# Kernel optimization log

Hardware: AMD Instinct MI355X
Metric: run time of the kernel (lower is better)

Reference implementation:

```python
import jax, jax.numpy as jnp
import numpy as np

D_MODEL = 1024; N_HEAD = 16; HD = 64
D_STATE = 128; D_CONV = 4; EXPAND = 2; HEADDIM = 64
D_INNER = EXPAND * D_MODEL          # 2048
NHEADS = D_INNER // HEADDIM         # 32
FFN = 4 * D_MODEL                   # 4096
B, T = 2, 1024


def rmsnorm(x, eps=1e-6):
    # FastSimpleRMSNorm: no learnable weight
    return x * jax.lax.rsqrt(jnp.mean(x * x, axis=-1, keepdims=True) + eps)


def causal_dwconv(x, w, b):
    # x: (..., T, C), w: (C, K), b: (C,). Causal depthwise conv (left pad K-1).
    K = w.shape[1]
    t = x.shape[-2]
    pad = [(0, 0)] * (x.ndim - 2) + [(K - 1, 0), (0, 0)]
    xp = jnp.pad(x, pad)
    y = jnp.zeros_like(x) + b
    for k in range(K):
        y = y + w[:, k] * jax.lax.slice_in_dim(xp, k, k + t, axis=-2)
    return y


def block_forward(x, W_in, conv_w, conv_b, A_log, Dm, dt_bias, mnorm_w, W_out,
                  W_qkv, W_cproj, qconv_w, qconv_b, kconv_w, kconv_b, vconv_w, vconv_b,
                  time_maa_k, time_maa_r, W_key, W_rec, W_val):
    Bsz, Tn, _ = x.shape
    # ---- Mamba2 branch ----
    h = rmsnorm(x)
    zxbcdt = h @ W_in                                  # (B,T,2*D_INNER+2*N+H)
    z = zxbcdt[..., :D_INNER]
    xBC = zxbcdt[..., D_INNER:2 * D_INNER + 2 * D_STATE]
    dt = zxbcdt[..., -NHEADS:]
    xBC = jax.nn.silu(causal_dwconv(xBC, conv_w, conv_b))
    xm = xBC[..., :D_INNER]
    Bm = xBC[..., D_INNER:D_INNER + D_STATE]           # (B,T,N)
    Cm = xBC[..., -D_STATE:]                           # (B,T,N)
    dt = jax.nn.softplus(dt + dt_bias)                 # (B,T,H)
    A = -jnp.exp(A_log)                                # (H,)
    xh = xm.reshape(Bsz, Tn, NHEADS, HEADDIM)          # (B,T,H,P)

    def step(hstate, inp):
        dt_t, x_t, B_t, C_t = inp                      # (B,H),(B,H,P),(B,N),(B,N)
        dA = jnp.exp(dt_t * A)                         # (B,H)
        hstate = hstate * dA[..., None, None] + (dt_t[..., None] * x_t)[..., None] * B_t[:, None, None, :]
        y_t = jnp.einsum('bhpn,bn->bhp', hstate, C_t)
        return hstate, y_t

    h0 = jnp.zeros((Bsz, NHEADS, HEADDIM, D_STATE), x.dtype)
    _, ys = jax.lax.scan(step, h0, (jnp.swapaxes(dt, 0, 1), jnp.swapaxes(xh, 0, 1),
                                    jnp.swapaxes(Bm, 0, 1), jnp.swapaxes(Cm, 0, 1)))
    y = jnp.swapaxes(ys, 0, 1) + xh * Dm[:, None]      # (B,T,H,P)
    y = y.reshape(Bsz, Tn, D_INNER) * jax.nn.silu(z)   # gated
    y = y * jax.lax.rsqrt(jnp.mean(y * y, axis=-1, keepdims=True) + 1e-5) * mnorm_w
    x = x + y @ W_out

    # ---- MQA with depthwise convs ----
    h = rmsnorm(x)
    qkv = h @ W_qkv                                    # (B,T,D_MODEL+2*HD)
    q = qkv[..., :D_MODEL].reshape(Bsz, Tn, N_HEAD, HD).transpose(0, 2, 1, 3)  # (B,H,T,D)
    k = qkv[..., D_MODEL:D_MODEL + HD]                 # (B,T,D) single kv head
    v = qkv[..., -HD:]
    q = causal_dwconv(q, qconv_w, qconv_b)
    k = causal_dwconv(k, kconv_w, kconv_b)
    v = causal_dwconv(v, vconv_w, vconv_b)
    scores = jnp.einsum('bhtd,bsd->bhts', q, k) / np.float32(np.sqrt(HD))
    mask = jnp.tril(jnp.ones((Tn, Tn), bool))
    scores = jnp.where(mask, scores, -jnp.inf)
    p = jax.nn.softmax(scores, axis=-1)
    y = jnp.einsum('bhts,bsd->bhtd', p, v)
    y = y.transpose(0, 2, 1, 3).reshape(Bsz, Tn, D_MODEL)
    x = x + y @ W_cproj

    # ---- RWKV CMix FFN ----
    h = rmsnorm(x)
    xx = jnp.pad(h, ((0, 0), (1, 0), (0, 0)))[:, :Tn] - h   # time_shift(x) - x
    xk = h + xx * time_maa_k
    xr = h + xx * time_maa_r
    kf = jnp.square(jax.nn.relu(xk @ W_key))           # ReLU^2
    kv = kf @ W_val
    x = x + jax.nn.sigmoid(xr @ W_rec) * kv
    return x


def setup_inputs() -> dict:
    key = jax.random.key(0)
    ks = jax.random.split(key, 16)
    def w(k, shape, sc=0.02):
        return jax.random.normal(k, shape, jnp.float32) * sc
    x = jax.random.normal(ks[0], (B, T, D_MODEL), jnp.float32)
    W_in = w(ks[1], (D_MODEL, 2 * D_INNER + 2 * D_STATE + NHEADS))
    conv_w = w(ks[2], (D_INNER + 2 * D_STATE, D_CONV), 0.2)
    conv_b = jnp.zeros((D_INNER + 2 * D_STATE,), jnp.float32)
    A_log = jnp.log(jnp.arange(1, NHEADS + 1, dtype=jnp.float32))
    Dm = jnp.ones((NHEADS,), jnp.float32)
    dt_bias = w(ks[3], (NHEADS,), 0.5)
    mnorm_w = jnp.ones((D_INNER,), jnp.float32)
    W_out = w(ks[4], (D_INNER, D_MODEL))
    W_qkv = w(ks[5], (D_MODEL, D_MODEL + 2 * HD))
    W_cproj = w(ks[6], (D_MODEL, D_MODEL))
    qconv_w = w(ks[7], (HD, 3), 0.3); qconv_b = jnp.zeros((HD,), jnp.float32)
    kconv_w = w(ks[8], (HD, 3), 0.3); kconv_b = jnp.zeros((HD,), jnp.float32)
    vconv_w = w(ks[9], (HD, 3), 0.3); vconv_b = jnp.zeros((HD,), jnp.float32)
    ddd = jnp.arange(D_MODEL, dtype=jnp.float32) / D_MODEL
    time_maa_k = 1.0 - ddd  # layer_id=0 -> ratio_1_to_almost0 = 1
    time_maa_r = 1.0 - ddd
    W_key = w(ks[10], (D_MODEL, FFN))
    W_rec = w(ks[11], (D_MODEL, D_MODEL))
    W_val = w(ks[12], (FFN, D_MODEL))
    return dict(x=x, W_in=W_in, conv_w=conv_w, conv_b=conv_b, A_log=A_log, Dm=Dm,
                dt_bias=dt_bias, mnorm_w=mnorm_w, W_out=W_out, W_qkv=W_qkv, W_cproj=W_cproj,
                qconv_w=qconv_w, qconv_b=qconv_b, kconv_w=kconv_w, kconv_b=kconv_b,
                vconv_w=vconv_w, vconv_b=vconv_b, time_maa_k=time_maa_k, time_maa_r=time_maa_r,
                W_key=W_key, W_rec=W_rec, W_val=W_val)


def reference(x, W_in, conv_w, conv_b, A_log, Dm, dt_bias, mnorm_w, W_out,
              W_qkv, W_cproj, qconv_w, qconv_b, kconv_w, kconv_b, vconv_w, vconv_b,
              time_maa_k, time_maa_r, W_key, W_rec, W_val):
    return block_forward(x, W_in, conv_w, conv_b, A_log, Dm, dt_bias, mnorm_w, W_out,
                         W_qkv, W_cproj, qconv_w, qconv_b, kconv_w, kconv_b, vconv_w, vconv_b,
                         time_maa_k, time_maa_r, W_key, W_rec, W_val)
```

## Files before the change

### kernel.cpp

```cpp
#include <hip/hip_runtime.h>
#include <hip/hip_bf16.h>
#include <math.h>

#define BB 2
#define TT 1024
#define BT (BB*TT)
#define DM 1024
#define DI 2048
#define DS 128
#define NHS 32
#define PDIM 64
#define NHA 16
#define HD 64
#define FFN_ 4096
#define NZX 4384
#define NXBC 2304
#define NXBCD 2336
#define CL 128
#define NC 8

typedef __hip_bfloat16 bf16;
typedef short bf16x8 __attribute__((ext_vector_type(8)));
typedef float f32x4 __attribute__((ext_vector_type(4)));

__device__ __forceinline__ float b2f(bf16 v){ return __bfloat162float(v); }
__device__ __forceinline__ bf16 f2b(float v){ return __float2bfloat16(v); }

__device__ __forceinline__ void gload16(const void* g, void* l) {
  __builtin_amdgcn_global_load_lds(
      (const __attribute__((address_space(1))) unsigned int*)g,
      (__attribute__((address_space(3))) unsigned int*)l,
      16, 0, 0);
}

__global__ void k_rms_in(const float* __restrict__ xin, float* __restrict__ X,
                         bf16* __restrict__ H) {
  int row = blockIdx.x;
  int tid = threadIdx.x;
  const float* xr = xin + (size_t)row * DM;
  float v[4]; float ss = 0.f;
  #pragma unroll
  for (int i = 0; i < 4; ++i) { v[i] = xr[tid*4+i]; ss += v[i]*v[i]; }
  __shared__ float red[256];
  red[tid] = ss; __syncthreads();
  for (int s = 128; s > 0; s >>= 1) { if (tid < s) red[tid] += red[tid+s]; __syncthreads(); }
  float scale = rsqrtf(red[0]/(float)DM + 1e-6f);
  float* Xr = X + (size_t)row*DM; bf16* Hr = H + (size_t)row*DM;
  #pragma unroll
  for (int i = 0; i < 4; ++i) { Xr[tid*4+i] = v[i]; Hr[tid*4+i] = f2b(v[i]*scale); }
}

__global__ void k_rms_f32(const float* __restrict__ X, bf16* __restrict__ H) {
  int row = blockIdx.x;
  int tid = threadIdx.x;
  const float* xr = X + (size_t)row * DM;
  float v[4]; float ss = 0.f;
  #pragma unroll
  for (int i = 0; i < 4; ++i) { v[i] = xr[tid*4+i]; ss += v[i]*v[i]; }
  __shared__ float red[256];
  red[tid] = ss; __syncthreads();
  for (int s = 128; s > 0; s >>= 1) { if (tid < s) red[tid] += red[tid+s]; __syncthreads(); }
  float scale = rsqrtf(red[0]/(float)DM + 1e-6f);
  bf16* Hr = H + (size_t)row*DM;
  #pragma unroll
  for (int i = 0; i < 4; ++i) Hr[tid*4+i] = f2b(v[i]*scale);
}

__global__ void k_rms_shift(const float* __restrict__ X, const float* __restrict__ maak,
                            const float* __restrict__ maar,
                            bf16* __restrict__ XK, bf16* __restrict__ XR) {
  int row = blockIdx.x; int t = row & (TT - 1);
  int tid = threadIdx.x;
  const float* xr = X + (size_t)row*DM;
  const float* xp = xr - DM;
  float v[4], pv[4]; float ss = 0.f, ssp = 0.f;
  #pragma unroll
  for (int i = 0; i < 4; ++i) {
    int c = tid*4 + i;
    v[i] = xr[c]; ss += v[i]*v[i];
    pv[i] = (t > 0) ? xp[c] : 0.f; ssp += pv[i]*pv[i];
  }
  __shared__ float red[256], red2[256];
  red[tid] = ss; red2[tid] = ssp; __syncthreads();
  for (int s = 128; s > 0; s >>= 1) {
    if (tid < s) { red[tid] += red[tid+s]; red2[tid] += red2[tid+s]; }
    __syncthreads();
  }
  float scale  = rsqrtf(red[0]/(float)DM + 1e-6f);
  float scalep = (t > 0) ? rsqrtf(red2[0]/(float)DM + 1e-6f) : 0.f;
  bf16* xk = XK + (size_t)row*DM; bf16* xrw = XR + (size_t)row*DM;
  #pragma unroll
  for (int i = 0; i < 4; ++i) {
    int c = tid*4 + i;
    float h = v[i]*scale;
    float xx = pv[i]*scalep - h;
    xk[c]  = f2b(h + xx*maak[c]);
    xrw[c] = f2b(h + xx*maar[c]);
  }
}

__global__ void k_tcast(const float* __restrict__ W, bf16* __restrict__ Wt,
                        int K, int N) {
  __shared__ float t[32][33];
  int tx = threadIdx.x, ty = threadIdx.y;
  int n0 = blockIdx.x*32, k0 = blockIdx.y*32;
  #pragma unroll
  for (int i = 0; i < 4; ++i) {
    int k = k0 + ty + i*8, n = n0 + tx;
    t[ty + i*8][tx] = (n < N) ? W[(size_t)k*N + n] : 0.f;
  }
  __syncthreads();
  #pragma unroll
  for (int i = 0; i < 4; ++i) {
    int n = n0 + ty + i*8, k = k0 + tx;
    Wt[(size_t)n*K + k] = f2b(t[tx][ty + i*8]);
  }
}

template<int EPI, bool ADD, bool OUTBF>
__global__ __launch_bounds__(256)
void mfma_gemm(const bf16* __restrict__ A, const bf16* __restrict__ Bt,
               float* __restrict__ C, bf16* __restrict__ Cbf,
               int M, int N, int K) {
  __shared__ bf16 As[128*32];
  __shared__ bf16 Bs[128*32];
  int tid = threadIdx.x;
  int wave = tid >> 6, lane = tid & 63;
  int m_l = lane & 15, quad = lane >> 4;
  int wr = (wave & 1) * 64, wc = (wave >> 1) * 64;
  int row0 = blockIdx.y * 128, col0 = blockIdx.x * 128;
  f32x4 acc[4][4];
  #pragma unroll
  for (int i = 0; i < 4; ++i)
    #pragma unroll
    for (int j = 0; j < 4; ++j) acc[i][j] = (f32x4){0.f,0.f,0.f,0.f};
  int lr = lane >> 2;
  int lc = (lane & 3) * 8;
  for (int k0 = 0; k0 < K; k0 += 32) {
    __syncthreads();
    #pragma unroll
    for (int g = 0; g < 2; ++g) {
      int rbase = 32*wave + 16*g;
      gload16(&A [(size_t)(row0 + rbase + lr)*K + k0 + lc], &As[rbase*32]);
      gload16(&Bt[(size_t)(col0 + rbase + lr)*K + k0 + lc], &Bs[rbase*32]);
    }
    __syncthreads();
    bf16x8 af[4], bfv[4];
    #pragma unroll
    for (int i = 0; i < 4; ++i) af[i]  = *(const bf16x8*)&As[(wr + i*16 + m_l)*32 + quad*8];
    #pragma unroll
    for (int j = 0; j < 4; ++j) bfv[j] = *(const bf16x8*)&Bs[(wc + j*16 + m_l)*32 + quad*8];
    #pragma unroll
    for (int i = 0; i < 4; ++i)
      #pragma unroll
      for (int j = 0; j < 4; ++j)
        acc[i][j] = __builtin_amdgcn_mfma_f32_16x16x32_bf16(af[i], bfv[j], acc[i][j], 0, 0, 0);
  }
  #pragma unroll
  for (int i = 0; i < 4; ++i) {
    #pragma unroll
    for (int j = 0; j < 4; ++j) {
      int col = col0 + wc + j*16 + m_l;
      if (col < N) {
        #pragma unroll
        for (int r = 0; r < 4; ++r) {
          int row = row0 + wr + i*16 + quad*4 + r;
          float v = acc[i][j][r];
          if (EPI == 1) { v = fmaxf(v, 0.f); v = v*v; }
          else if (EPI == 2) v = 1.f/(1.f + __expf(-v));
          if (OUTBF)      Cbf[(size_t)row*N + col] = f2b(v);
          else if (ADD)   C[(size_t)row*N + col] += v;
          else            C[(size_t)row*N + col]  = v;
        }
      }
    }
  }
}

__global__ __launch_bounds__(256)
void mfma_sk32(const bf16* __restrict__ A, const bf16* __restrict__ Bt,
               float* __restrict__ P0, float* __restrict__ P1,
               float* __restrict__ P2, float* __restrict__ P3,
               int M, int N, int K, int kchunk) {
  __shared__ bf16 As[128*32];
  __shared__ bf16 Bs[128*32];
  int tid = threadIdx.x;
  int wave = tid >> 6, lane = tid & 63;
  int m_l = lane & 15, quad = lane >> 4;
  int wr = (wave & 1) * 64, wc = (wave >> 1) * 64;
  int row0 = blockIdx.y * 128, col0 = blockIdx.x * 128;
  int kbeg = blockIdx.z * kchunk;
  int kend = kbeg + kchunk;
  f32x4 acc[4][4];
  #pragma unroll
  for (int i = 0; i < 4; ++i)
    #pragma unroll
    for (int j = 0; j < 4; ++j) acc[i][j] = (f32x4){0.f,0.f,0.f,0.f};
  int lr = lane >> 2;
  int lc = (lane & 3) * 8;
  for (int k0 = kbeg; k0 < kend; k0 += 32) {
    __syncthreads();
    #pragma unroll
    for (int g = 0; g < 2; ++g) {
      int rbase = 32*wave + 16*g;
      gload16(&A [(size_t)(row0 + rbase + lr)*K + k0 + lc], &As[rbase*32]);
      gload16(&Bt[(size_t)(col0 + rbase + lr)*K + k0 + lc], &Bs[rbase*32]);
    }
    __syncthreads();
    bf16x8 af[4], bfv[4];
    #pragma unroll
    for (int i = 0; i < 4; ++i) af[i]  = *(const bf16x8*)&As[(wr + i*16 + m_l)*32 + quad*8];
    #pragma unroll
    for (int j = 0; j < 4; ++j) bfv[j] = *(const bf16x8*)&Bs[(wc + j*16 + m_l)*32 + quad*8];
    #pragma unroll
    for (int i = 0; i < 4; ++i)
      #pragma unroll
      for (int j = 0; j < 4; ++j)
        acc[i][j] = __builtin_amdgcn_mfma_f32_16x16x32_bf16(af[i], bfv[j], acc[i][j], 0, 0, 0);
  }
  float* P = (blockIdx.z == 0) ? P0 : (blockIdx.z == 1) ? P1 : (blockIdx.z == 2) ? P2 : P3;
  #pragma unroll
  for (int i = 0; i < 4; ++i) {
    #pragma unroll
    for (int j = 0; j < 4; ++j) {
      int col = col0 + wc + j*16 + m_l;
      if (col < N) {
        #pragma unroll
        for (int r = 0; r < 4; ++r) {
          int row = row0 + wr + i*16 + quad*4 + r;
          P[(size_t)row*N + col] = acc[i][j][r];
        }
      }
    }
  }
}

template<int Z, int EPI, bool ADD>
__global__ void k_reduce(float* __restrict__ dst, const float* __restrict__ p0,
                         const float* __restrict__ p1, const float* __restrict__ p2,
                         const float* __restrict__ p3) {
  size_t i = ((size_t)blockIdx.x*256 + threadIdx.x)*4;
  float4 a = *(const float4*)(p0 + i);
  float4 b = *(const float4*)(p1 + i);
  float r0 = a.x + b.x, r1 = a.y + b.y, r2 = a.z + b.z, r3 = a.w + b.w;
  if (Z == 4) {
    float4 c = *(const float4*)(p2 + i);
    float4 d = *(const float4*)(p3 + i);
    r0 += c.x + d.x; r1 += c.y + d.y; r2 += c.z + d.z; r3 += c.w + d.w;
  }
  if (EPI == 2) {
    r0 = 1.f/(1.f + __expf(-r0)); r1 = 1.f/(1.f + __expf(-r1));
    r2 = 1.f/(1.f + __expf(-r2)); r3 = 1.f/(1.f + __expf(-r3));
  }
  if (ADD) {
    float4 o = *(const float4*)(dst + i);
    r0 += o.x; r1 += o.y; r2 += o.z; r3 += o.w;
  }
  float4 res; res.x = r0; res.y = r1; res.z = r2; res.w = r3;
  *(float4*)(dst + i) = res;
}

__global__ void k_reduce_final(const float* __restrict__ p0, const float* __restrict__ p1,
                               const float* __restrict__ X, const float* __restrict__ KV,
                               float* __restrict__ out) {
  size_t i = ((size_t)blockIdx.x*256 + threadIdx.x)*4;
  float4 a = *(const float4*)(p0 + i);
  float4 b = *(const float4*)(p1 + i);
  float4 x = *(const float4*)(X + i);
  float4 kv = *(const float4*)(KV + i);
  float r0 = 1.f/(1.f + __expf(-(a.x + b.x)));
  float r1 = 1.f/(1.f + __expf(-(a.y + b.y)));
  float r2 = 1.f/(1.f + __expf(-(a.z + b.z)));
  float r3 = 1.f/(1.f + __expf(-(a.w + b.w)));
  float4 res;
  res.x = x.x + r0*kv.x; res.y = x.y + r1*kv.y;
  res.z = x.z + r2*kv.z; res.w = x.w + r3*kv.w;
  *(float4*)(out + i) = res;
}

__global__ void k_conv_ssm(const float* __restrict__ ZXr, const float* __restrict__ cw,
                           const float* __restrict__ cb, const float* __restrict__ dtb,
                           bf16* __restrict__ XBCb, float* __restrict__ DT) {
  int bt = blockIdx.x; int b = bt >> 10; int t = bt & 1023;
  int tid = threadIdx.x;
  for (int c = tid; c < NXBC; c += 256) {
    float acc = cb[c];
    #pragma unroll
    for (int kk = 0; kk < 4; ++kk) {
      int ts = t - 3 + kk;
      if (ts >= 0) acc += cw[c*4+kk] * ZXr[((size_t)(b*TT+ts))*NXBCD + c];
    }
    float s = acc / (1.f + __expf(-acc));
    XBCb[(size_t)bt*NXBC + c] = f2b(s);
  }
  if (tid < NHS) {
    float x = ZXr[(size_t)bt*NXBCD + NXBC + tid] + dtb[tid];
    float sp = (x > 20.f) ? x : log1pf(__expf(x));
    DT[(size_t)bt*NHS + tid] = sp;
  }
}

__global__ __launch_bounds__(512)
void k_scan1(const bf16* __restrict__ xbcb, const float* __restrict__ dt,
             const float* __restrict__ A_log, const float* __restrict__ Dmv,
             float* __restrict__ Y, float* __restrict__ SC, float* __restrict__ CUM) {
  int bc = blockIdx.x;
  int bh = bc >> 3, c = bc & 7;
  int b = bh >> 5, h = bh & 31;
  int tid = threadIdx.x, wave = tid >> 6, lane = tid & 63;
  int col = lane & 15, quad = lane >> 4;
  int t0 = c * CL;
  __shared__ bf16 sB[128*136];
  __shared__ bf16 sC[128*136];
  __shared__ bf16 sxT[64*136];
  __shared__ float sL[128], sdt[128], sW[128];
  float A = -__expf(A_log[h]);
  float Dmh = Dmv[h];
  for (int e = tid; e < 128*16; e += 512) {
    int r = e >> 4, ch = e & 15;
    const bf16* row = xbcb + (size_t)(b*TT + t0 + r)*NXBC;
    *(uint4*)&sB[r*136 + ch*8] = *(const uint4*)&row[2048 + ch*8];
    *(uint4*)&sC[r*136 + ch*8] = *(const uint4*)&row[2176 + ch*8];
  }
  for (int e = tid; e < 64*128; e += 512) {
    int p = e & 63, t = e >> 6;
    sxT[p*136 + t] = xbcb[(size_t)(b*TT + t0 + t)*NXBC + h*64 + p];
  }
  if (tid < 128) sdt[tid] = dt[(size_t)(b*TT + t0 + tid)*NHS + h];
  __syncthreads();
  if (wave == 0) {
    float a0 = sdt[2*lane]*A, a1 = sdt[2*lane+1]*A;
    float tot = a0 + a1;
    #pragma unroll
    for (int off = 1; off < 64; off <<= 1) {
      float up = __shfl_up(tot, off);
      if (lane >= off) tot += up;
    }
    sL[2*lane+1] = tot;
    sL[2*lane]   = tot - a1;
  }
  __syncthreads();
  int wr = (wave & 1)*64, wc = (wave >> 1)*32;
  f32x4 g[4][2];
  #pragma unroll
  for (int i = 0; i < 4; ++i)
    #pragma unroll
    for (int j = 0; j < 2; ++j) g[i][j] = (f32x4){0.f,0.f,0.f,0.f};
  #pragma unroll
  for (int kf = 0; kf < 4; ++kf) {
    bf16x8 af[4], bfr[2];
    #pragma unroll
    for (int i = 0; i < 4; ++i) af[i]  = *(const bf16x8*)&sC[(wr + i*16 + col)*136 + kf*32 + quad*8];
    #pragma unroll
    for (int j = 0; j < 2; ++j) bfr[j] = *(const bf16x8*)&sB[(wc + j*16 + col)*136 + kf*32 + quad*8];
    #pragma unroll
    for (int i = 0; i < 4; ++i)
      #pragma unroll
      for (int j = 0; j < 2; ++j)
        g[i][j] = __builtin_amdgcn_mfma_f32_16x16x32_bf16(af[i], bfr[j], g[i][j], 0, 0, 0);
  }
  float Lend = sL[127];
  if (tid < 128) sW[tid] = __expf(Lend - sL[tid]) * sdt[tid];
  __syncthreads();
  if (tid < 128) CUM[(size_t)bh*TT + t0 + tid] = __expf(sL[tid]);
  #pragma unroll
  for (int i = 0; i < 4; ++i) {
    #pragma unroll
    for (int j = 0; j < 2; ++j) {
      int sl = wc + j*16 + col;
      #pragma unroll
      for (int r = 0; r < 4; ++r) {
        int tl = wr + i*16 + quad*4 + r;
        float v = (sl <= tl) ? g[i][j][r] * __expf(sL[tl] - sL[sl]) * sdt[sl] : 0.f;
        sC[tl*136 + sl] = f2b(v);
      }
    }
  }
  for (int e = tid; e < 128*128; e += 512) {
    int n = e & 127, s = e >> 7;
    sB[n*136 + s] = f2b(b2f(xbcb[(size_t)(b*TT + t0 + s)*NXBC + 2048 + n]) * sW[s]);
  }
  __syncthreads();
  int tb = (wave & 3)*32, pb = (wave >> 2)*32;
  f32x4 ya[2][2];
  #pragma unroll
  for (int i2 = 0; i2 < 2; ++i2)
    #pragma unroll
    for (int jd = 0; jd < 2; ++jd) ya[i2][jd] = (f32x4){0.f,0.f,0.f,0.f};
  #pragma unroll
  for (int kf = 0; kf < 4; ++kf) {
    bf16x8 pa[2], xa[2];
    #pragma unroll
    for (int i2 = 0; i2 < 2; ++i2)
      pa[i2] = *(const bf16x8*)&sC[(tb + i2*16 + col)*136 + kf*32 + quad*8];
    #pragma unroll
    for (int jd = 0; jd < 2; ++jd)
      xa[jd] = *(const bf16x8*)&sxT[(pb + jd*16 + col)*136 + kf*32 + quad*8];
    #pragma unroll
    for (int i2 = 0; i2 < 2; ++i2)
      #pragma unroll
      for (int jd = 0; jd < 2; ++jd)
        ya[i2][jd] = __builtin_amdgcn_mfma_f32_16x16x32_bf16(pa[i2], xa[jd], ya[i2][jd], 0, 0, 0);
  }
  #pragma unroll
  for (int i2 = 0; i2 < 2; ++i2) {
    #pragma unroll
    for (int jd = 0; jd < 2; ++jd) {
      int p = pb + jd*16 + col;
      #pragma unroll
      for (int r = 0; r < 4; ++r) {
        int tl = tb + i2*16 + quad*4 + r;
        float xv = b2f(sxT[p*136 + tl]);
        Y[(size_t)(b*TT + t0 + tl)*DI + h*64 + p] = ya[i2][jd][r] + xv*Dmh;
      }
    }
  }
  int pb3 = (wave & 3)*16, nb = (wave >> 2)*64;
  f32x4 sa[4];
  #pragma unroll
  for (int nt = 0; nt < 4; ++nt) sa[nt] = (f32x4){0.f,0.f,0.f,0.f};
  #pragma unroll
  for (int kf = 0; kf < 4; ++kf) {
    bf16x8 xpa = *(const bf16x8*)&sxT[(pb3 + col)*136 + kf*32 + quad*8];
    #pragma unroll
    for (int nt = 0; nt < 4; ++nt) {
      bf16x8 bwa = *(const bf16x8*)&sB[(nb + nt*16 + col)*136 + kf*32 + quad*8];
      sa[nt] = __builtin_amdgcn_mfma_f32_16x16x32_bf16(xpa, bwa, sa[nt], 0, 0, 0);
    }
  }
  #pragma unroll
  for (int nt = 0; nt < 4; ++nt) {
    int n = nb + nt*16 + col;
    #pragma unroll
    for (int r = 0; r < 4; ++r) {
      int p = pb3 + quad*4 + r;
      SC[((size_t)(bh*NC + c)*64 + p)*128 + n] = sa[nt][r];
    }
  }
}

__global__ __launch_bounds__(512)
void k_scan2(float* __restrict__ SC, const float* __restrict__ CUM) {
  int bh = blockIdx.x;
  int tid = threadIdx.x;
  int p = tid >> 3, g = tid & 7;
  float S[16];
  #pragma unroll
  for (int j = 0; j < 16; ++j) S[j] = 0.f;
  for (int c = 0; c < NC; ++c) {
    size_t base = ((size_t)(bh*NC + c)*64 + p)*128 + g*16;
    float Ptot = CUM[(size_t)bh*TT + c*CL + (CL-1)];
    float tmp[16];
    #pragma unroll
    for (int j = 0; j < 16; ++j) tmp[j] = SC[base + j];
    #pragma unroll
    for (int j = 0; j < 16; ++j) SC[base + j] = S[j];
    #pragma unroll
    for (int j = 0; j < 16; ++j) S[j] = S[j]*Ptot + tmp[j];
  }
}

__global__ __launch_bounds__(256)
void k_scan3(const bf16* __restrict__ xbcb, const float* __restrict__ SC,
             const float* __restrict__ CUM, float* __restrict__ Y) {
  int bc = blockIdx.x;
  int bh = bc >> 3, c = bc & 7;
  if (c == 0) return;
  int b = bh >> 5, h = bh & 31;
  int tid = threadIdx.x, wave = tid >> 6, lane = tid & 63;
  int col = lane & 15, quad = lane >> 4;
  int t0 = c * CL;
  __shared__ bf16 sCt[128*136];
  __shared__ bf16 sS[64*136];
  __shared__ float sCum[128];
  for (int e = tid; e < 128*16; e += 256) {
    int r = e >> 4, ch = e & 15;
    *(uint4*)&sCt[r*136 + ch*8] =
      *(const uint4*)&xbcb[(size_t)(b*TT + t0 + r)*NXBC + 2176 + ch*8];
  }
  for (int e = tid; e < 64*128; e += 256) {
    int n = e & 127, p = e >> 7;
    sS[p*136 + n] = f2b(SC[((size_t)(bh*NC + c)*64 + p)*128 + n]);
  }
  if (tid < 128) sCum[tid] = CUM[(size_t)bh*TT + t0 + tid];
  __syncthreads();
  f32x4 ya[2][4];
  #pragma unroll
  for (int i2 = 0; i2 < 2; ++i2)
    #pragma unroll
    for (int jd = 0; jd < 4; ++jd) ya[i2][jd] = (f32x4){0.f,0.f,0.f,0.f};
  #pragma unroll
  for (int kf = 0; kf < 4; ++kf) {
    bf16x8 pa[2], sv[4];
    #pragma unroll
    for (int i2 = 0; i2 < 2; ++i2)
      pa[i2] = *(const bf16x8*)&sCt[(wave*32 + i2*16 + col)*136 + kf*32 + quad*8];
    #pragma unroll
    for (int jd = 0; jd < 4; ++jd)
      sv[jd] = *(const bf16x8*)&sS[(jd*16 + col)*136 + kf*32 + quad*8];
    #pragma unroll
    for (int i2 = 0; i2 < 2; ++i2)
      #pragma unroll
      for (int jd = 0; jd < 4; ++jd)
        ya[i2][jd] = __builtin_amdgcn_mfma_f32_16x16x32_bf16(pa[i2], sv[jd], ya[i2][jd], 0, 0, 0);
  }
  #pragma unroll
  for (int i2 = 0; i2 < 2; ++i2) {
    #pragma unroll
    for (int jd = 0; jd < 4; ++jd) {
      int p = jd*16 + col;
      #pragma unroll
      for (int r = 0; r < 4; ++r) {
        int tl = wave*32 + i2*16 + quad*4 + r;
        Y[(size_t)(b*TT + t0 + tl)*DI + h*64 + p] += sCum[tl]*ya[i2][jd][r];
      }
    }
  }
}

__global__ void k_gate(const float* __restrict__ Y, const float* __restrict__ Z,
                       const float* __restrict__ mnw, bf16* __restrict__ Ybf) {
  int row = blockIdx.x; int tid = threadIdx.x;
  const float* yr = Y + (size_t)row*DI;
  const float* zr = Z + (size_t)row*DI;
  float gv[8]; float ss = 0.f;
  #pragma unroll
  for (int i = 0; i < 8; ++i) {
    int c = tid*8 + i;
    float z = zr[c];
    float sz = z / (1.f + __expf(-z));
    float v = yr[c]*sz;
    gv[i] = v; ss += v*v;
  }
  __shared__ float red[256];
  red[tid] = ss; __syncthreads();
  for (int s = 128; s > 0; s >>= 1) { if (tid < s) red[tid] += red[tid+s]; __syncthreads(); }
  float scale = rsqrtf(red[0]/(float)DI + 1e-5f);
  bf16* br = Ybf + (size_t)row*DI;
  #pragma unroll
  for (int i = 0; i < 8; ++i) { int c = tid*8 + i; br[c] = f2b(gv[i]*scale*mnw[c]); }
}

__global__ void k_conv_qkv(const float* __restrict__ QKV,
                           const float* qw, const float* qb, const float* kw, const float* kb,
                           const float* vw, const float* vb,
                           bf16* __restrict__ Qb, bf16* __restrict__ Kb, bf16* __restrict__ Vtb) {
  int bt = blockIdx.x; int b = bt >> 10; int t = bt & 1023;
  int tid = threadIdx.x;
  for (int c = tid; c < 1152; c += 256) {
    if (c < 1024) {
      int h = c >> 6, d = c & 63;
      float acc = qb[d];
      #pragma unroll
      for (int kk = 0; kk < 3; ++kk) { int ts = t-2+kk; if (ts >= 0) acc += qw[d*3+kk] * QKV[((size_t)(b*TT+ts))*1152 + c]; }
      Qb[((size_t)(b*NHA + h)*TT + t)*HD + d] = f2b(acc * 0.125f);
    } else if (c < 1088) {
      int d = c - 1024;
      float acc = kb[d];
      #pragma unroll
      for (int kk = 0; kk < 3; ++kk) { int ts = t-2+kk; if (ts >= 0) acc += kw[d*3+kk] * QKV[((size_t)(b*TT+ts))*1152 + c]; }
      Kb[(size_t)bt*HD + d] = f2b(acc);
    } else {
      int d = c - 1088;
      float acc = vb[d];
      #pragma unroll
      for (int kk = 0; kk < 3; ++kk) { int ts = t-2+kk; if (ts >= 0) acc += vw[d*3+kk] * QKV[((size_t)(b*TT+ts))*1152 + c]; }
      Vtb[((size_t)(b*HD + d))*TT + t] = f2b(acc);
    }
  }
}

__global__ __launch_bounds__(256)
void k_flash_sk(const bf16* __restrict__ Qb, const bf16* __restrict__ Kb,
                const bf16* __restrict__ Vtb, float* __restrict__ Op,
                float* __restrict__ Lp) {
  int qt = blockIdx.x >> 1, z = blockIdx.x & 1;
  int h = blockIdx.y, b = blockIdx.z;
  int n = qt + 1;
  int kmid = (n + 1) >> 1;
  int kbeg = z ? kmid : 0;
  int kend = z ? n : kmid;
  int tid = threadIdx.x, wave = tid >> 6, lane = tid & 63;
  int col = lane & 15, quad = lane >> 4;
  int t0 = qt * 128;
  __shared__ bf16 Ks[128*72];
  __shared__ bf16 Vs[64*136];
  __shared__ bf16 Ps[4][32*136];
  const bf16* Qbase = Qb + ((size_t)(b*NHA + h))*TT*HD;
  float lst[2][4];
  f32x4 oacc[2][4];
  #pragma unroll
  for (int i = 0; i < 2; ++i)
    #pragma unroll
    for (int r = 0; r < 4; ++r) lst[i][r] = 0.f;
  #pragma unroll
  for (int i = 0; i < 2; ++i)
    #pragma unroll
    for (int jd = 0; jd < 4; ++jd) oacc[i][jd] = (f32x4){0.f,0.f,0.f,0.f};
  if (kbeg < kend) {
    bf16x8 qf[2][2];
    #pragma unroll
    for (int i = 0; i < 2; ++i)
      #pragma unroll
      for (int kf = 0; kf < 2; ++kf)
        qf[i][kf] = *(const bf16x8*)&Qbase[(size_t)(t0 + wave*32 + i*16 + col)*HD + kf*32 + quad*8];

    for (int kt = kbeg; kt < kend; ++kt) {
      int s0 = kt * 128;
      __syncthreads();
      for (int e = tid; e < 1024; e += 256) {
        int r = e >> 3, ch = e & 7;
        *(uint4*)&Ks[r*72 + ch*8] = *(const uint4*)&Kb[((size_t)(b*TT + s0 + r))*HD + ch*8];
      }
      for (int e = tid; e < 1024; e += 256) {
        int d = e >> 4, ch = e & 15;
        *(uint4*)&Vs[d*136 + ch*8] = *(const uint4*)&Vtb[((size_t)(b*HD + d))*TT + s0 + ch*8];
      }
      __syncthreads();
      f32x4 sacc[2][8];
      #pragma unroll
      for (int i = 0; i < 2; ++i)
        #pragma unroll
        for (int j = 0; j < 8; ++j) sacc[i][j] = (f32x4){0.f,0.f,0.f,0.f};
      __builtin_amdgcn_s_setprio(1);
      #pragma unroll
      for (int j = 0; j < 8; ++j) {
        bf16x8 kf0 = *(const bf16x8*)&Ks[(j*16 + col)*72 + quad*8];
        bf16x8 kf1 = *(const bf16x8*)&Ks[(j*16 + col)*72 + 32 + quad*8];
        #pragma unroll
        for (int i = 0; i < 2; ++i) {
          sacc[i][j] = __builtin_amdgcn_mfma_f32_16x16x32_bf16(qf[i][0], kf0, sacc[i][j], 0, 0, 0);
          sacc[i][j] = __builtin_amdgcn_mfma_f32_16x16x32_bf16(qf[i][1], kf1, sacc[i][j], 0, 0, 0);
        }
      }
      __builtin_amdgcn_s_setprio(0);
      bool diag = (kt == qt);
      #pragma unroll
      for (int i = 0; i < 2; ++i) {
        #pragma unroll
        for (int r = 0; r < 4; ++r) {
          int rowloc = wave*32 + i*16 + quad*4 + r;
          #pragma unroll
          for (int j = 0; j < 8; ++j) {
            float pv = __expf(sacc[i][j][r]);
            if (diag && (j*16 + col > rowloc)) pv = 0.f;
            sacc[i][j][r] = pv;
            lst[i][r] += pv;
          }
        }
      }
      #pragma unroll
      for (int i = 0; i < 2; ++i)
        #pragma unroll
        for (int j = 0; j < 8; ++j)
          #pragma unroll
          for (int r = 0; r < 4; ++r)
            Ps[wave][(i*16 + quad*4 + r)*136 + j*16 + col] = f2b(sacc[i][j][r]);
      __builtin_amdgcn_s_setprio(1);
      #pragma unroll
      for (int i = 0; i < 2; ++i) {
        bf16x8 pa[4];
        #pragma unroll
        for (int kf = 0; kf < 4; ++kf)
          pa[kf] = *(const bf16x8*)&Ps[wave][(i*16 + col)*136 + kf*32 + quad*8];
        #pragma unroll
        for (int jd = 0; jd < 4; ++jd) {
          #pragma unroll
          for (int kf = 0; kf < 4; ++kf) {
            bf16x8 vbf = *(const bf16x8*)&Vs[(jd*16 + col)*136 + kf*32 + quad*8];
            oacc[i][jd] = __builtin_amdgcn_mfma_f32_16x16x32_bf16(pa[kf], vbf, oacc[i][jd], 0, 0, 0);
          }
        }
      }
      __builtin_amdgcn_s_setprio(0);
    }
    #pragma unroll
    for (int i = 0; i < 2; ++i)
      #pragma unroll
      for (int r = 0; r < 4; ++r) {
        float l = lst[i][r];
        l += __shfl_xor(l, 1);
        l += __shfl_xor(l, 2);
        l += __shfl_xor(l, 4);
        l += __shfl_xor(l, 8);
        lst[i][r] = l;
      }
  }
  if (qt == 0 && z == 1) return;
  size_t robase = ((size_t)((z*BB + b)*NHA + h))*TT + t0;
  #pragma unroll
  for (int i = 0; i < 2; ++i) {
    #pragma unroll
    for (int jd = 0; jd < 4; ++jd) {
      int d = jd*16 + col;
      #pragma unroll
      for (int r = 0; r < 4; ++r) {
        int tl = wave*32 + i*16 + quad*4 + r;
        Op[(robase + tl)*HD + d] = oacc[i][jd][r];
      }
    }
  }
  if (col == 0) {
    #pragma unroll
    for (int i = 0; i < 2; ++i)
      #pragma unroll
      for (int r = 0; r < 4; ++r) {
        int tl = wave*32 + i*16 + quad*4 + r;
        Lp[robase + tl] = lst[i][r];
      }
  }
}

__global__ void k_att_comb(const float* __restrict__ Op, const float* __restrict__ Lp,
                           bf16* __restrict__ outb) {
  int idx = blockIdx.x*256 + threadIdx.x;
  int e = idx*4;
  int c = e & (DM - 1); int h = c >> 6; int d = c & 63;
  int bt = e >> 10; int t = bt & (TT - 1); int b = bt >> 10;
  int qt = t >> 7;
  size_t r0 = ((size_t)(b*NHA + h))*TT + t;
  float4 o0 = *(const float4*)&Op[r0*HD + d];
  float l = Lp[r0];
  float ox = o0.x, oy = o0.y, oz = o0.z, ow = o0.w;
  if (qt > 0) {
    size_t r1 = ((size_t)((BB + b)*NHA + h))*TT + t;
    float4 o1 = *(const float4*)&Op[r1*HD + d];
    l += Lp[r1];
    ox += o1.x; oy += o1.y; oz += o1.z; ow += o1.w;
  }
  float inv = 1.f / l;
  bf16* p = outb + (size_t)bt*DM + c;
  p[0] = f2b(ox*inv); p[1] = f2b(oy*inv); p[2] = f2b(oz*inv); p[3] = f2b(ow*inv);
}

extern "C" void kernel_launch(void* const* d_in, const int* in_sizes, int n_in,
                              void* d_out, int out_size, void* d_ws, size_t ws_size,
                              hipStream_t stream) {
  const float* x_in    = (const float*)d_in[0];
  const float* W_in    = (const float*)d_in[1];
  const float* conv_w  = (const float*)d_in[2];
  const float* conv_b  = (const float*)d_in[3];
  const float* A_log   = (const float*)d_in[4];
  const float* Dm      = (const float*)d_in[5];
  const float* dt_bias = (const float*)d_in[6];
  const float* mnorm_w = (const float*)d_in[7];
  const float* W_out   = (const float*)d_in[8];
  const float* W_qkv   = (const float*)d_in[9];
  const float* W_cproj = (const float*)d_in[10];
  const float* qconv_w = (const float*)d_in[11];
  const float* qconv_b = (const float*)d_in[12];
  const float* kconv_w = (const float*)d_in[13];
  const float* kconv_b = (const float*)d_in[14];
  const float* vconv_w = (const float*)d_in[15];
  const float* vconv_b = (const float*)d_in[16];
  const float* maa_k   = (const float*)d_in[17];
  const float* maa_r   = (const float*)d_in[18];
  const float* W_key   = (const float*)d_in[19];
  const float* W_rec   = (const float*)d_in[20];
  const float* W_val   = (const float*)d_in[21];
  float* out = (float*)d_out;

  float* ws = (float*)d_ws;
  float* X       = ws;
  bf16*  Hbf     = (bf16*)(ws + 2097152);
  float* Zbuf    = ws + 3145728;
  float* XBCDraw = ws + 7340032;
  float* XBC     = ws + 12124160;
  float* DT      = ws + 16842752;
  float* CUM     = ws + 16908288;
  float* Y       = ws + 16973824;

  bf16*  Wt_in    = (bf16*)XBC;
  bf16*  XBCb     = (bf16*)XBC;
  float* SC       = XBCDraw;
  bf16*  Ybf      = (bf16*)XBC;
  bf16*  Wt_out   = (bf16*)(XBC + 2097152);
  float* QKV      = Zbuf;
  bf16*  Wt_qkv   = (bf16*)XBC;
  bf16*  Qb       = (bf16*)XBCDraw;
  bf16*  Kb       = (bf16*)(XBCDraw + 1048576);
  bf16*  Vtb      = (bf16*)(XBCDraw + 1114112);
  bf16*  ATTNbf   = (bf16*)Y;
  bf16*  Wt_cproj = (bf16*)(Y + 1048576);
  bf16*  XKbf     = (bf16*)XBC;
  bf16*  XRbf     = (bf16*)(XBC + 1048576);
  bf16*  Wt_key   = (bf16*)Zbuf;
  bf16*  KFbf     = (bf16*)XBCDraw;
  bf16*  Wt_val   = (bf16*)Zbuf;
  float* KV       = Y;
  bf16*  Wt_rec   = (bf16*)Zbuf;
  float* FOp      = Zbuf;
  float* FLp      = ws + 2097152;

  dim3 thr256(256), thr512(512);
  dim3 tblk(32, 8);

  k_rms_in<<<BT, thr256, 0, stream>>>(x_in, X, Hbf);
  k_tcast<<<dim3(4480/32, 1024/32), tblk, 0, stream>>>(W_in, Wt_in, 1024, NZX);
  mfma_gemm<0,false,false><<<dim3(16, 16), thr256, 0, stream>>>(Hbf, Wt_in, Zbuf, nullptr, BT, 2048, 1024);
  mfma_gemm<0,false,false><<<dim3(19, 16), thr256, 0, stream>>>(Hbf, Wt_in + (size_t)2048*1024, XBCDraw, nullptr, BT, NXBCD, 1024);
  k_conv_ssm<<<BT, thr256, 0, stream>>>(XBCDraw, conv_w, conv_b, dt_bias, XBCb, DT);
  k_scan1<<<BB*NHS*NC, thr512, 0, stream>>>(XBCb, DT, A_log, Dm, Y, SC, CUM);
  k_scan2<<<BB*NHS, thr512, 0, stream>>>(SC, CUM);
  k_scan3<<<BB*NHS*NC, thr256, 0, stream>>>(XBCb, SC, CUM, Y);
  k_gate<<<BT, thr256, 0, stream>>>(Y, Zbuf, mnorm_w, Ybf);
  k_tcast<<<dim3(1024/32, 2048/32), tblk, 0, stream>>>(W_out, Wt_out, 2048, 1024);
  mfma_sk32<<<dim3(8, 16, 4), thr256, 0, stream>>>(Ybf, Wt_out,
      Zbuf, Zbuf + 2097152, XBCDraw, XBCDraw + 2097152, BT, 1024, 2048, 512);
  k_reduce<4,0,true><<<2048, thr256, 0, stream>>>(X, Zbuf, Zbuf + 2097152, XBCDraw, XBCDraw + 2097152);
  k_rms_f32<<<BT, thr256, 0, stream>>>(X, Hbf);
  k_tcast<<<dim3(1152/32, 1024/32), tblk, 0, stream>>>(W_qkv, Wt_qkv, 1024, 1152);
  mfma_sk32<<<dim3(9, 16, 2), thr256, 0, stream>>>(Hbf, Wt_qkv,
      XBCDraw, XBCDraw + 2359296, XBCDraw, XBCDraw, BT, 1152, 1024, 512);
  k_reduce<2,0,false><<<2304, thr256, 0, stream>>>(QKV, XBCDraw, XBCDraw + 2359296, XBCDraw, XBCDraw);
  k_conv_qkv<<<BT, thr256, 0, stream>>>(QKV, qconv_w, qconv_b, kconv_w, kconv_b, vconv_w, vconv_b, Qb, Kb, Vtb);
  k_flash_sk<<<dim3((TT/128)*2, NHA, BB), thr256, 0, stream>>>(Qb, Kb, Vtb, FOp, FLp);
  k_att_comb<<<(BT*DM)/(256*4), thr256, 0, stream>>>(FOp, FLp, ATTNbf);
  k_tcast<<<dim3(1024/32, 1024/32), tblk, 0, stream>>>(W_cproj, Wt_cproj, 1024, 1024);
  mfma_sk32<<<dim3(8, 16, 2), thr256, 0, stream>>>(ATTNbf, Wt_cproj,
      XBC, XBC + 2097152, XBC, XBC, BT, 1024, 1024, 512);
  k_reduce<2,0,true><<<2048, thr256, 0, stream>>>(X, XBC, XBC + 2097152, XBC, XBC);
  k_rms_shift<<<BT, thr256, 0, stream>>>(X, maa_k, maa_r, XKbf, XRbf);
  k_tcast<<<dim3(4096/32, 1024/32), tblk, 0, stream>>>(W_key, Wt_key, 1024, 4096);
  mfma_gemm<1,false,true><<<dim3(32, 16), thr256, 0, stream>>>(XKbf, Wt_key, nullptr, KFbf, BT, 4096, 1024);
  k_tcast<<<dim3(1024/32, 4096/32), tblk, 0, stream>>>(W_val, Wt_val, 4096, 1024);
  mfma_sk32<<<dim3(8, 16, 4), thr256, 0, stream>>>(KFbf, Wt_val,
      Y, Y + 2097152, XBC + 2621440, Zbuf + 2097152, BT, 1024, 4096, 1024);
  k_reduce<4,0,false><<<2048, thr256, 0, stream>>>(KV, Y, Y + 2097152, XBC + 2621440, Zbuf + 2097152);
  k_tcast<<<dim3(1024/32, 1024/32), tblk, 0, stream>>>(W_rec, Wt_rec, 1024, 1024);
  mfma_sk32<<<dim3(8, 16, 2), thr256, 0, stream>>>(XRbf, Wt_rec,
      Y + 2097152, XBC + 2621440, Y, Y, BT, 1024, 1024, 512);
  k_reduce_final<<<2048, thr256, 0, stream>>>(Y + 2097152, XBC + 2621440, X, KV, out);
}
```

Baseline: 541.3 us.

## Fuse split-K reductions into RMSNorm and final epilogue; use 8-wave flash attention

Folds the 4-way split-K reduction of the Mamba output projection into the following RMSNorm, removing one kernel and a round-trip of X. It also drops the separate KV reduction and sums the four value-projection partials inside the final sigmoid-gate epilogue. Scratch buffers are reassigned so those partials stay live until the end. The flash attention kernel moves from 4 waves with 32 query rows each to 8 waves with 16 rows each, which adds parallelism per block but makes each wave reuse its K/V tile less.

Result: faster. 524.8 us (-3.0%).

```diff
diff --git a/kernel.cpp b/kernel.cpp
--- a/kernel.cpp
+++ b/kernel.cpp
@@ -50,20 +50,31 @@
   for (int i = 0; i < 4; ++i) { Xr[tid*4+i] = v[i]; Hr[tid*4+i] = f2b(v[i]*scale); }
 }
 
-__global__ void k_rms_f32(const float* __restrict__ X, bf16* __restrict__ H) {
-  int row = blockIdx.x;
-  int tid = threadIdx.x;
-  const float* xr = X + (size_t)row * DM;
-  float v[4]; float ss = 0.f;
-  #pragma unroll
-  for (int i = 0; i < 4; ++i) { v[i] = xr[tid*4+i]; ss += v[i]*v[i]; }
+__global__ void k_reduce4_rms(const float* __restrict__ p0, const float* __restrict__ p1,
+                              const float* __restrict__ p2, const float* __restrict__ p3,
+                              float* __restrict__ X, bf16* __restrict__ H) {
+  int row = blockIdx.x; int tid = threadIdx.x;
+  size_t base = (size_t)row*DM + tid*4;
+  float4 a = *(const float4*)(p0 + base);
+  float4 b = *(const float4*)(p1 + base);
+  float4 c = *(const float4*)(p2 + base);
+  float4 d = *(const float4*)(p3 + base);
+  float4 x = *(const float4*)(X + base);
+  float v[4];
+  v[0] = x.x + a.x + b.x + c.x + d.x;
+  v[1] = x.y + a.y + b.y + c.y + d.y;
+  v[2] = x.z + a.z + b.z + c.z + d.z;
+  v[3] = x.w + a.w + b.w + c.w + d.w;
+  float ss = v[0]*v[0] + v[1]*v[1] + v[2]*v[2] + v[3]*v[3];
   __shared__ float red[256];
   red[tid] = ss; __syncthreads();
   for (int s = 128; s > 0; s >>= 1) { if (tid < s) red[tid] += red[tid+s]; __syncthreads(); }
   float scale = rsqrtf(red[0]/(float)DM + 1e-6f);
-  bf16* Hr = H + (size_t)row*DM;
-  #pragma unroll
-  for (int i = 0; i < 4; ++i) Hr[tid*4+i] = f2b(v[i]*scale);
+  float4 res; res.x = v[0]; res.y = v[1]; res.z = v[2]; res.w = v[3];
+  *(float4*)(X + base) = res;
+  bf16* Hr = H + (size_t)row*DM + tid*4;
+  #pragma unroll
+  for (int i = 0; i < 4; ++i) Hr[i] = f2b(v[i]*scale);
 }
 
 __global__ void k_rms_shift(const float* __restrict__ X, const float* __restrict__ maak,
@@ -260,21 +271,27 @@
   *(float4*)(dst + i) = res;
 }
 
-__global__ void k_reduce_final(const float* __restrict__ p0, const float* __restrict__ p1,
-                               const float* __restrict__ X, const float* __restrict__ KV,
-                               float* __restrict__ out) {
+__global__ void k_reduce_final6(const float* __restrict__ k0, const float* __restrict__ k1,
+                                const float* __restrict__ k2, const float* __restrict__ k3,
+                                const float* __restrict__ r0p, const float* __restrict__ r1p,
+                                const float* __restrict__ X, float* __restrict__ out) {
   size_t i = ((size_t)blockIdx.x*256 + threadIdx.x)*4;
-  float4 a = *(const float4*)(p0 + i);
-  float4 b = *(const float4*)(p1 + i);
+  float4 a = *(const float4*)(k0 + i);
+  float4 b = *(const float4*)(k1 + i);
+  float4 c = *(const float4*)(k2 + i);
+  float4 d = *(const float4*)(k3 + i);
+  float4 ra = *(const float4*)(r0p + i);
+  float4 rb = *(const float4*)(r1p + i);
   float4 x = *(const float4*)(X + i);
-  float4 kv = *(const float4*)(KV + i);
-  float r0 = 1.f/(1.f + __expf(-(a.x + b.x)));
-  float r1 = 1.f/(1.f + __expf(-(a.y + b.y)));
-  float r2 = 1.f/(1.f + __expf(-(a.z + b.z)));
-  float r3 = 1.f/(1.f + __expf(-(a.w + b.w)));
+  float kvx = a.x + b.x + c.x + d.x, kvy = a.y + b.y + c.y + d.y;
+  float kvz = a.z + b.z + c.z + d.z, kvw = a.w + b.w + c.w + d.w;
+  float sx = 1.f/(1.f + __expf(-(ra.x + rb.x)));
+  float sy = 1.f/(1.f + __expf(-(ra.y + rb.y)));
+  float sz = 1.f/(1.f + __expf(-(ra.z + rb.z)));
+  float sw = 1.f/(1.f + __expf(-(ra.w + rb.w)));
   float4 res;
-  res.x = x.x + r0*kv.x; res.y = x.y + r1*kv.y;
-  res.z = x.z + r2*kv.z; res.w = x.w + r3*kv.w;
+  res.x = x.x + sx*kvx; res.y = x.y + sy*kvy;
+  res.z = x.z + sz*kvz; res.w = x.w + sw*kvw;
   *(float4*)(out + i) = res;
 }
 
@@ -570,7 +587,7 @@
   }
 }
 
-__global__ __launch_bounds__(256)
+__global__ __launch_bounds__(512)
 void k_flash_sk(const bf16* __restrict__ Qb, const bf16* __restrict__ Kb,
                 const bf16* __restrict__ Vtb, float* __restrict__ Op,
                 float* __restrict__ Lp) {
@@ -585,129 +602,103 @@
   int t0 = qt * 128;
   __shared__ bf16 Ks[128*72];
   __shared__ bf16 Vs[64*136];
-  __shared__ bf16 Ps[4][32*136];
+  __shared__ bf16 Ps[8][16*136];
   const bf16* Qbase = Qb + ((size_t)(b*NHA + h))*TT*HD;
-  float lst[2][4];
-  f32x4 oacc[2][4];
-  #pragma unroll
-  for (int i = 0; i < 2; ++i)
-    #pragma unroll
-    for (int r = 0; r < 4; ++r) lst[i][r] = 0.f;
-  #pragma unroll
-  for (int i = 0; i < 2; ++i)
-    #pragma unroll
-    for (int jd = 0; jd < 4; ++jd) oacc[i][jd] = (f32x4){0.f,0.f,0.f,0.f};
+  float lst[4];
+  f32x4 oacc[4];
+  #pragma unroll
+  for (int r = 0; r < 4; ++r) lst[r] = 0.f;
+  #pragma unroll
+  for (int jd = 0; jd < 4; ++jd) oacc[jd] = (f32x4){0.f,0.f,0.f,0.f};
   if (kbeg < kend) {
-    bf16x8 qf[2][2];
-    #pragma unroll
-    for (int i = 0; i < 2; ++i)
-      #pragma unroll
-      for (int kf = 0; kf < 2; ++kf)
-        qf[i][kf] = *(const bf16x8*)&Qbase[(size_t)(t0 + wave*32 + i*16 + col)*HD + kf*32 + quad*8];
+    bf16x8 qf[2];
+    #pragma unroll
+    for (int kf = 0; kf < 2; ++kf)
+      qf[kf] = *(const bf16x8*)&Qbase[(size_t)(t0 + wave*16 + col)*HD + kf*32 + quad*8];
 
     for (int kt = kbeg; kt < kend; ++kt) {
       int s0 = kt * 128;
       __syncthreads();
-      for (int e = tid; e < 1024; e += 256) {
+      for (int e = tid; e < 1024; e += 512) {
         int r = e >> 3, ch = e & 7;
         *(uint4*)&Ks[r*72 + ch*8] = *(const uint4*)&Kb[((size_t)(b*TT + s0 + r))*HD + ch*8];
       }
-      for (int e = tid; e < 1024; e += 256) {
+      for (int e = tid; e < 1024; e += 512) {
         int d = e >> 4, ch = e & 15;
         *(uint4*)&Vs[d*136 + ch*8] = *(const uint4*)&Vtb[((size_t)(b*HD + d))*TT + s0 + ch*8];
       }
       __syncthreads();
-      f32x4 sacc[2][8];
-      #pragma unroll
-      for (int i = 0; i < 2; ++i)
-        #pragma unroll
-        for (int j = 0; j < 8; ++j) sacc[i][j] = (f32x4){0.f,0.f,0.f,0.f};
+      f32x4 sacc[8];
+      #pragma unroll
+      for (int j = 0; j < 8; ++j) sacc[j] = (f32x4){0.f,0.f,0.f,0.f};
       __builtin_amdgcn_s_setprio(1);
       #pragma unroll
       for (int j = 0; j < 8; ++j) {
         bf16x8 kf0 = *(const bf16x8*)&Ks[(j*16 + col)*72 + quad*8];
         bf16x8 kf1 = *(const bf16x8*)&Ks[(j*16 + col)*72 + 32 + quad*8];
-        #pragma unroll
-        for (int i = 0; i < 2; ++i) {
-          sacc[i][j] = __builtin_amdgcn_mfma_f32_16x16x32_bf16(qf[i][0], kf0, sacc[i][j], 0, 0, 0);
-          sacc[i][j] = __builtin_amdgcn_mfma_f32_16x16x32_bf16(qf[i][1], kf1, sacc[i][j], 0, 0, 0);
-        }
+        sacc[j] = __builtin_amdgcn_mfma_f32_16x16x32_bf16(qf[0], kf0, sacc[j], 0, 0, 0);
+        sacc[j] = __builtin_amdgcn_mfma_f32_16x16x32_bf16(qf[1], kf1, sacc[j], 0, 0, 0);
       }
       __builtin_amdgcn_s_setprio(0);
       bool diag = (kt == qt);
       #pragma unroll
-      for (int i = 0; i < 2; ++i) {
+      for (int r = 0; r < 4; ++r) {
+        int rowloc = wave*16 + quad*4 + r;
         #pragma unroll
-        for (int r = 0; r < 4; ++r) {
-          int rowloc = wave*32 + i*16 + quad*4 + r;
-          #pragma unroll
-          for (int j = 0; j < 8; ++j) {
-            float pv = __expf(sacc[i][j][r]);
-            if (diag && (j*16 + col > rowloc)) pv = 0.f;
-            sacc[i][j][r] = pv;
-            lst[i][r] += pv;
-          }
+        for (int j = 0; j < 8; ++j) {
+          float pv = __expf(sacc[j][r]);
+          if (diag && (j*16 + col > rowloc)) pv = 0.f;
+          sacc[j][r] = pv;
+          lst[r] += pv;
         }
       }
       #pragma unroll
-      for (int i = 0; i < 2; ++i)
+      for (int j = 0; j < 8; ++j)
         #pragma unroll
-        for (int j = 0; j < 8; ++j)
-          #pragma unroll
-          for (int r = 0; r < 4; ++r)
-            Ps[wave][(i*16 + quad*4 + r)*136 + j*16 + col] = f2b(sacc[i][j][r]);
+        for (int r = 0; r < 4; ++r)
+          Ps[wave][(quad*4 + r)*136 + j*16 + col] = f2b(sacc[j][r]);
       __builtin_amdgcn_s_setprio(1);
-      #pragma unroll
-      for (int i = 0; i < 2; ++i) {
-        bf16x8 pa[4];
+      bf16x8 pa[4];
+      #pragma unroll
+      for (int kf = 0; kf < 4; ++kf)
+        pa[kf] = *(const bf16x8*)&Ps[wave][col*136 + kf*32 + quad*8];
+      #pragma unroll
+      for (int jd = 0; jd < 4; ++jd) {
         #pragma unroll
-        for (int kf = 0; kf < 4; ++kf)
-          pa[kf] = *(const bf16x8*)&Ps[wave][(i*16 + col)*136 + kf*32 + quad*8];
-        #pragma unroll
-        for (int jd = 0; jd < 4; ++jd) {
-          #pragma unroll
-          for (int kf = 0; kf < 4; ++kf) {
-            bf16x8 vbf = *(const bf16x8*)&Vs[(jd*16 + col)*136 + kf*32 + quad*8];
-            oacc[i][jd] = __builtin_amdgcn_mfma_f32_16x16x32_bf16(pa[kf], vbf, oacc[i][jd], 0, 0, 0);
-          }
+        for (int kf = 0; kf < 4; ++kf) {
+          bf16x8 vbf = *(const bf16x8*)&Vs[(jd*16 + col)*136 + kf*32 + quad*8];
+          oacc[jd] = __builtin_amdgcn_mfma_f32_16x16x32_bf16(pa[kf], vbf, oacc[jd], 0, 0, 0);
         }
       }
       __builtin_amdgcn_s_setprio(0);
     }
     #pragma unroll
-    for (int i = 0; i < 2; ++i)
-      #pragma unroll
-      for (int r = 0; r < 4; ++r) {
-        float l = lst[i][r];
-        l += __shfl_xor(l, 1);
-        l += __shfl_xor(l, 2);
-        l += __shfl_xor(l, 4);
-        l += __shfl_xor(l, 8);
-        lst[i][r] = l;
-      }
+    for (int r = 0; r < 4; ++r) {
+      float l = lst[r];
+      l += __shfl_xor(l, 1);
+      l += __shfl_xor(l, 2);
+      l += __shfl_xor(l, 4);
+      l += __shfl_xor(l, 8);
+      lst[r] = l;
+    }
   }
   if (qt == 0 && z == 1) return;
   size_t robase = ((size_t)((z*BB + b)*NHA + h))*TT + t0;
   #pragma unroll
-  for (int i = 0; i < 2; ++i) {
-    #pragma unroll
-    for (int jd = 0; jd < 4; ++jd) {
-      int d = jd*16 + col;
-      #pragma unroll
-      for (int r = 0; r < 4; ++r) {
-        int tl = wave*32 + i*16 + quad*4 + r;
-        Op[(robase + tl)*HD + d] = oacc[i][jd][r];
-      }
+  for (int jd = 0; jd < 4; ++jd) {
+    int d = jd*16 + col;
+    #pragma unroll
+    for (int r = 0; r < 4; ++r) {
+      int tl = wave*16 + quad*4 + r;
+      Op[(robase + tl)*HD + d] = oacc[jd][r];
     }
   }
   if (col == 0) {
     #pragma unroll
-    for (int i = 0; i < 2; ++i)
-      #pragma unroll
-      for (int r = 0; r < 4; ++r) {
-        int tl = wave*32 + i*16 + quad*4 + r;
-        Lp[robase + tl] = lst[i][r];
-      }
+    for (int r = 0; r < 4; ++r) {
+      int tl = wave*16 + quad*4 + r;
+      Lp[robase + tl] = lst[r];
+    }
   }
 }
 
@@ -787,7 +778,6 @@
   bf16*  Wt_key   = (bf16*)Zbuf;
   bf16*  KFbf     = (bf16*)XBCDraw;
   bf16*  Wt_val   = (bf16*)Zbuf;
-  float* KV       = Y;
   bf16*  Wt_rec   = (bf16*)Zbuf;
   float* FOp      = Zbuf;
   float* FLp      = ws + 2097152;
@@ -807,28 +797,28 @@
   k_tcast<<<dim3(1024/32, 2048/32), tblk, 0, stream>>>(W_out, Wt_out, 2048, 1024);
   mfma_sk32<<<dim3(8, 16, 4), thr256, 0, stream>>>(Ybf, Wt_out,
       Zbuf, Zbuf + 2097152, XBCDraw, XBCDraw + 2097152, BT, 1024, 2048, 512);
-  k_reduce<4,0,true><<<2048, thr256, 0, stream>>>(X, Zbuf, Zbuf + 2097152, XBCDraw, XBCDraw + 2097152);
-  k_rms_f32<<<BT, thr256, 0, stream>>>(X, Hbf);
+  k_reduce4_rms<<<BT, thr256, 0, stream>>>(Zbuf, Zbuf + 2097152, XBCDraw, XBCDraw + 2097152, X, Hbf);
   k_tcast<<<dim3(1152/32, 1024/32), tblk, 0, stream>>>(W_qkv, Wt_qkv, 1024, 1152);
   mfma_sk32<<<dim3(9, 16, 2), thr256, 0, stream>>>(Hbf, Wt_qkv,
       XBCDraw, XBCDraw + 2359296, XBCDraw, XBCDraw, BT, 1152, 1024, 512);
   k_reduce<2,0,false><<<2304, thr256, 0, stream>>>(QKV, XBCDraw, XBCDraw + 2359296, XBCDraw, XBCDraw);
   k_conv_qkv<<<BT, thr256, 0, stream>>>(QKV, qconv_w, qconv_b, kconv_w, kconv_b, vconv_w, vconv_b, Qb, Kb, Vtb);
-  k_flash_sk<<<dim3((TT/128)*2, NHA, BB), thr256, 0, stream>>>(Qb, Kb, Vtb, FOp, FLp);
+  k_flash_sk<<<dim3((TT/128)*2, NHA, BB), thr512, 0, stream>>>(Qb, Kb, Vtb, FOp, FLp);
   k_att_comb<<<(BT*DM)/(256*4), thr256, 0, stream>>>(FOp, FLp, ATTNbf);
   k_tcast<<<dim3(1024/32, 1024/32), tblk, 0, stream>>>(W_cproj, Wt_cproj, 1024, 1024);
   mfma_sk32<<<dim3(8, 16, 2), thr256, 0, stream>>>(ATTNbf, Wt_cproj,
-      XBC, XBC + 2097152, XBC, XBC, BT, 1024, 1024, 512);
-  k_reduce<2,0,true><<<2048, thr256, 0, stream>>>(X, XBC, XBC + 2097152, XBC, XBC);
+      Zbuf, Zbuf + 2097152, Zbuf, Zbuf, BT, 1024, 1024, 512);
+  k_reduce<2,0,true><<<2048, thr256, 0, stream>>>(X, Zbuf, Zbuf + 2097152, Zbuf, Zbuf);
   k_rms_shift<<<BT, thr256, 0, stream>>>(X, maa_k, maa_r, XKbf, XRbf);
   k_tcast<<<dim3(4096/32, 1024/32), tblk, 0, stream>>>(W_key, Wt_key, 1024, 4096);
   mfma_gemm<1,false,true><<<dim3(32, 16), thr256, 0, stream>>>(XKbf, Wt_key, nullptr, KFbf, BT, 4096, 1024);
   k_tcast<<<dim3(1024/32, 4096/32), tblk, 0, stream>>>(W_val, Wt_val, 4096, 1024);
   mfma_sk32<<<dim3(8, 16, 4), thr256, 0, stream>>>(KFbf, Wt_val,
       Y, Y + 2097152, XBC + 2621440, Zbuf + 2097152, BT, 1024, 4096, 1024);
-  k_reduce<4,0,false><<<2048, thr256, 0, stream>>>(KV, Y, Y + 2097152, XBC + 2621440, Zbuf + 2097152);
   k_tcast<<<dim3(1024/32, 1024/32), tblk, 0, stream>>>(W_rec, Wt_rec, 1024, 1024);
   mfma_sk32<<<dim3(8, 16, 2), thr256, 0, stream>>>(XRbf, Wt_rec,
-      Y + 2097152, XBC + 2621440, Y, Y, BT, 1024, 1024, 512);
-  k_reduce_final<<<2048, thr256, 0, stream>>>(Y + 2097152, XBC + 2621440, X, KV, out);
-}
+      XBCDraw, XBCDraw + 2097152, XBCDraw, XBCDraw, BT, 1024, 1024, 512);
+  k_reduce_final6<<<2048, thr256, 0, stream>>>(
+      Y, Y + 2097152, XBC + 2621440, Zbuf + 2097152,
+      XBCDraw, XBCDraw + 2097152, X, out);
+}
```
